# Kernel optimization log

Hardware: AMD Instinct MI355X
Metric: run time of the kernel (lower is better)

The kernel has to match this reference:

```python
import jax, jax.numpy as jnp
import numpy as np

DIM = 768
HEADS = 12
DH = DIM // HEADS  # 64


def setup_inputs() -> dict:
    key = jax.random.key(0)
    k1, k2, k3, k4, k5 = jax.random.split(key, 5)
    b, p = 16, 1024
    x = jax.random.normal(k1, (b, p, DIM), dtype=jnp.float32)
    # torch nn.Linear params: W [out, in], b [out]
    s_qkv = 1.0 / np.sqrt(DIM)
    Wqkv = jax.random.uniform(k2, (3 * DIM, DIM), jnp.float32, -s_qkv, s_qkv)
    bqkv = jax.random.uniform(k3, (3 * DIM,), jnp.float32, -s_qkv, s_qkv)
    Wo = jax.random.uniform(k4, (DIM, DIM), jnp.float32, -s_qkv, s_qkv)
    bo = jax.random.uniform(k5, (DIM,), jnp.float32, -s_qkv, s_qkv)
    return {"x": x, "Wqkv": Wqkv, "bqkv": bqkv, "Wo": Wo, "bo": bo}


def reference(x, Wqkv, bqkv, Wo, bo):
    b, p, _ = x.shape
    qkv = x @ Wqkv.T + bqkv                      # [b, p, 3*dim]
    q, k, v = jnp.split(qkv, 3, axis=-1)
    def to_heads(t):
        return t.reshape(b, p, HEADS, DH).transpose(0, 2, 1, 3)  # [b, h, p, d]
    q, k, v = to_heads(q), to_heads(k), to_heads(v)
    A = jnp.einsum('bhqd,bhkd->bhqk', q, k) / jnp.sqrt(jnp.float32(DH))
    # NOTE: softmax over the QUERY axis (dim=2), not the key axis
    P = jax.nn.softmax(A, axis=2)                # [b, h, q, k]
    MSA = jnp.einsum('bhqk,bhkd->bhqd', P, v)    # [b, h, p, d]
    MSA = MSA.transpose(0, 2, 1, 3).reshape(b, p, DIM)
    return MSA @ Wo.T + bo
```

## Files before the change

### kernel.cpp

```cpp
#include <hip/hip_runtime.h>
#include <hip/hip_bf16.h>
#include <math.h>

#define DIMC 768
#define HEADS 12
#define DHD 64
#define NB 16
#define NP 1024
#define NQKV (3*DIMC)

typedef __attribute__((ext_vector_type(8))) short bf16x8;
typedef __attribute__((ext_vector_type(4))) float f32x4;

__device__ __forceinline__ short f2bf(float f){
  unsigned u = __builtin_bit_cast(unsigned, f);
  u = (u + 0x7fffu + ((u >> 16) & 1u)) >> 16;
  return (short)u;
}
__device__ __forceinline__ float bf2f(short s){
  return __builtin_bit_cast(float, ((unsigned)(unsigned short)s) << 16);
}
__device__ __forceinline__ bf16x8 cvt8(float4 a, float4 b){
  bf16x8 v;
  v[0]=f2bf(a.x); v[1]=f2bf(a.y); v[2]=f2bf(a.z); v[3]=f2bf(a.w);
  v[4]=f2bf(b.x); v[5]=f2bf(b.y); v[6]=f2bf(b.z); v[7]=f2bf(b.w);
  return v;
}
__device__ __forceinline__ void glds16(const void* gsrc, void* ldst){
  __builtin_amdgcn_global_load_lds(
      (const __attribute__((address_space(1))) unsigned int*)gsrc,
      (__attribute__((address_space(3))) unsigned int*)ldst, 16, 0, 0);
}

__global__ __launch_bounds__(256) void cvt_bf16(const float* __restrict__ in, short* __restrict__ out, int n8)
{
  int i = blockIdx.x*256 + threadIdx.x;
  if (i < n8) {
    float4 f0 = ((const float4*)in)[i*2];
    float4 f1 = ((const float4*)in)[i*2+1];
    ((bf16x8*)out)[i] = cvt8(f0, f1);
  }
}

template<int BCVT, int OUTBF16>
__global__ __launch_bounds__(256) void gemm_bt(
    const short* __restrict__ A, const void* __restrict__ Bp,
    const float* __restrict__ bias, void* __restrict__ Cp,
    int N, int K)
{
  __shared__ __align__(16) short As[128*32];
  __shared__ __align__(16) short Bs[128*32];
  const int bn = blockIdx.x * 128, bm = blockIdx.y * 128;
  const int t = threadIdx.x;
  const int lane = t & 63, w = t >> 6;
  const int wr = w >> 1, wc = w & 1;
  const int lr = lane & 15, lg = lane >> 4;
  const int srow = lane >> 2;
  const int acol = (lane & 3) * 8;

  f32x4 acc[4][4] = {};

  for (int k0 = 0; k0 < K; k0 += 32) {
    glds16(A + (size_t)(bm + w*32 +  0 + srow)*K + k0 + acol, &As[(w*32 +  0)*32]);
    glds16(A + (size_t)(bm + w*32 + 16 + srow)*K + k0 + acol, &As[(w*32 + 16)*32]);
    if (BCVT) {
      const float* wp = (const float*)Bp + (size_t)(bn + (t>>1))*K + k0 + (t&1)*16;
      float4 f0 = ((const float4*)wp)[0];
      float4 f1 = ((const float4*)wp)[1];
      float4 f2 = ((const float4*)wp)[2];
      float4 f3 = ((const float4*)wp)[3];
      *(bf16x8*)&Bs[(t>>1)*32 + (t&1)*16]     = cvt8(f0, f1);
      *(bf16x8*)&Bs[(t>>1)*32 + (t&1)*16 + 8] = cvt8(f2, f3);
    } else {
      const short* bq = (const short*)Bp;
      glds16(bq + (size_t)(bn + w*32 +  0 + srow)*K + k0 + acol, &Bs[(w*32 +  0)*32]);
      glds16(bq + (size_t)(bn + w*32 + 16 + srow)*K + k0 + acol, &Bs[(w*32 + 16)*32]);
    }
    __syncthreads();
    bf16x8 a[4], b[4];
    #pragma unroll
    for (int i=0;i<4;i++) a[i] = *(const bf16x8*)&As[(wr*64 + i*16 + lr)*32 + lg*8];
    #pragma unroll
    for (int i=0;i<4;i++) b[i] = *(const bf16x8*)&Bs[(wc*64 + i*16 + lr)*32 + lg*8];
    #pragma unroll
    for (int mf=0;mf<4;mf++)
      #pragma unroll
      for (int nf=0;nf<4;nf++)
        acc[mf][nf] = __builtin_amdgcn_mfma_f32_16x16x32_bf16(a[mf], b[nf], acc[mf][nf], 0,0,0);
    __syncthreads();
  }
  #pragma unroll
  for (int nf=0;nf<4;nf++){
    const int n = bn + wc*64 + nf*16 + lr;
    const float bb = bias[n];
    #pragma unroll
    for (int mf=0;mf<4;mf++)
      #pragma unroll
      for (int i=0;i<4;i++){
        const int m = bm + wr*64 + mf*16 + lg*4 + i;
        const float v = acc[mf][nf][i] + bb;
        if (OUTBF16) ((short*)Cp)[(size_t)m*N + n] = f2bf(v);
        else         ((float*)Cp)[(size_t)m*N + n] = v;
      }
  }
}

__global__ __launch_bounds__(256) void vtrans(const short* __restrict__ qkv,
                                              const float* __restrict__ invs,
                                              short* __restrict__ vT)
{
  __shared__ __align__(16) short Ts[64][72];
  __shared__ float invl[64];
  const int pt = blockIdx.x, h = blockIdx.y, b = blockIdx.z;
  const int t = threadIdx.x;
  const size_t bh = (size_t)(b*HEADS + h);
  if (t < 64) invl[t] = invs[bh*NP + pt*64 + t];
  {
    const int r = t >> 2, q = t & 3;
    const short* src = qkv + (size_t)(b*NP + pt*64 + r)*NQKV + 2*DIMC + h*DHD + q*16;
    *(bf16x8*)&Ts[r][q*16]   = *(const bf16x8*)src;
    *(bf16x8*)&Ts[r][q*16+8] = *(const bf16x8*)(src+8);
  }
  __syncthreads();
  {
    const int d = t >> 2, q = t & 3;
    __align__(16) short tmp[16];
    #pragma unroll
    for (int j=0;j<16;j++) tmp[j] = f2bf(bf2f(Ts[q*16 + j][d]) * invl[q*16 + j]);
    short* dst = vT + (bh*DHD + d)*NP + pt*64 + q*16;
    *(bf16x8*)dst     = *(bf16x8*)&tmp[0];
    *(bf16x8*)(dst+8) = *(bf16x8*)&tmp[8];
  }
}

__global__ __launch_bounds__(256) void col_stats(const short* __restrict__ qkv, float* __restrict__ invs)
{
  __shared__ __align__(16) short Ks[128][72];
  __shared__ __align__(16) short Qs[64][72];
  __shared__ float red[4][128];
  const int kc = blockIdx.x, h = blockIdx.y, b = blockIdx.z;
  const int t = threadIdx.x;
  const int lane = t & 63, w = t >> 6;
  const int lr = lane & 15, lg = lane >> 4, lk = lg*8;
  const size_t rowbase = (size_t)(b*NP)*NQKV + h*DHD;
  {
    const int r = t >> 1, half = t & 1;
    const short* src = qkv + rowbase + (size_t)(kc*128 + r)*NQKV + DIMC + half*32;
    #pragma unroll
    for (int c=0;c<4;c++)
      *(bf16x8*)&Ks[r][half*32 + c*8] = *(const bf16x8*)(src + c*8);
  }
  float rsum[8] = {};
  for (int qt=0; qt<16; qt++){
    __syncthreads();
    {
      const int r = t >> 2, q = t & 3;
      const short* src = qkv + rowbase + (size_t)(qt*64 + r)*NQKV + q*16;
      *(bf16x8*)&Qs[r][q*16]   = *(const bf16x8*)src;
      *(bf16x8*)&Qs[r][q*16+8] = *(const bf16x8*)(src+8);
    }
    __syncthreads();
    bf16x8 qa0 = *(const bf16x8*)&Qs[w*16 + lr][lk];
    bf16x8 qa1 = *(const bf16x8*)&Qs[w*16 + lr][32 + lk];
    #pragma unroll
    for (int kf=0; kf<8; kf++){
      f32x4 acc = {};
      bf16x8 kb0 = *(const bf16x8*)&Ks[kf*16 + lr][lk];
      bf16x8 kb1 = *(const bf16x8*)&Ks[kf*16 + lr][32 + lk];
      acc = __builtin_amdgcn_mfma_f32_16x16x32_bf16(qa0, kb0, acc, 0,0,0);
      acc = __builtin_amdgcn_mfma_f32_16x16x32_bf16(qa1, kb1, acc, 0,0,0);
      #pragma unroll
      for (int i=0;i<4;i++) rsum[kf] += __expf(acc[i] * 0.125f);
    }
  }
  #pragma unroll
  for (int kf=0;kf<8;kf++){
    float v = rsum[kf];
    v += __shfl_xor(v, 16);
    v += __shfl_xor(v, 32);
    if (lane < 16) red[w][kf*16 + lr] = v;
  }
  __syncthreads();
  if (t < 128) {
    float s = red[0][t] + red[1][t] + red[2][t] + red[3][t];
    invs[(size_t)(b*HEADS + h)*NP + kc*128 + t] = 1.0f / s;
  }
}

__global__ __launch_bounds__(256) void attn_pv(const short* __restrict__ qkv, const short* __restrict__ vT,
                                               short* __restrict__ msa)
{
  __shared__ __align__(16) short Qs[64][72];
  __shared__ __align__(16) short Ks[64][72];
  __shared__ __align__(16) short Vs[64][72];
  __shared__ __align__(16) short Ps[4][16][72];
  const int qt = blockIdx.x, h = blockIdx.y, b = blockIdx.z;
  const int t = threadIdx.x;
  const int lane = t & 63, w = t >> 6;
  const int lr = lane & 15, lg = lane >> 4, lk = lg*8;
  const size_t qkvbase = (size_t)(b*NP)*NQKV + h*DHD;
  const size_t bh = (size_t)(b*HEADS + h);
  {
    const int r = t >> 2, q = t & 3;
    const short* src = qkv + qkvbase + (size_t)(qt*64 + r)*NQKV + q*16;
    *(bf16x8*)&Qs[r][q*16]   = *(const bf16x8*)src;
    *(bf16x8*)&Qs[r][q*16+8] = *(const bf16x8*)(src+8);
  }
  __syncthreads();
  bf16x8 qa0 = *(const bf16x8*)&Qs[w*16 + lr][lk];
  bf16x8 qa1 = *(const bf16x8*)&Qs[w*16 + lr][32 + lk];
  f32x4 o[4] = {};
  for (int kt=0; kt<16; kt++){
    __syncthreads();
    {
      const int r = t >> 2, q = t & 3;
      const short* ksrc = qkv + qkvbase + (size_t)(kt*64 + r)*NQKV + DIMC + q*16;
      *(bf16x8*)&Ks[r][q*16]   = *(const bf16x8*)ksrc;
      *(bf16x8*)&Ks[r][q*16+8] = *(const bf16x8*)(ksrc+8);
      const short* vsrc = vT + (bh*DHD + r)*NP + kt*64 + q*16;
      *(bf16x8*)&Vs[r][q*16]   = *(const bf16x8*)vsrc;
      *(bf16x8*)&Vs[r][q*16+8] = *(const bf16x8*)(vsrc+8);
    }
    __syncthreads();
    f32x4 s[4];
    #pragma unroll
    for (int kf=0;kf<4;kf++){
      f32x4 a = {};
      bf16x8 kb0 = *(const bf16x8*)&Ks[kf*16 + lr][lk];
      bf16x8 kb1 = *(const bf16x8*)&Ks[kf*16 + lr][32 + lk];
      a = __builtin_amdgcn_mfma_f32_16x16x32_bf16(qa0, kb0, a, 0,0,0);
      a = __builtin_amdgcn_mfma_f32_16x16x32_bf16(qa1, kb1, a, 0,0,0);
      s[kf] = a;
    }
    #pragma unroll
    for (int kf=0;kf<4;kf++){
      #pragma unroll
      for (int i=0;i<4;i++){
        const float p = __expf(s[kf][i]*0.125f);
        Ps[w][lg*4 + i][kf*16 + lr] = f2bf(p);
      }
    }
    __syncthreads();
    bf16x8 pa0 = *(const bf16x8*)&Ps[w][lr][lk];
    bf16x8 pa1 = *(const bf16x8*)&Ps[w][lr][32 + lk];
    #pragma unroll
    for (int df=0;df<4;df++){
      bf16x8 vb0 = *(const bf16x8*)&Vs[df*16 + lr][lk];
      bf16x8 vb1 = *(const bf16x8*)&Vs[df*16 + lr][32 + lk];
      o[df] = __builtin_amdgcn_mfma_f32_16x16x32_bf16(pa0, vb0, o[df], 0,0,0);
      o[df] = __builtin_amdgcn_mfma_f32_16x16x32_bf16(pa1, vb1, o[df], 0,0,0);
    }
  }
  #pragma unroll
  for (int df=0;df<4;df++){
    const int d = h*DHD + df*16 + lr;
    #pragma unroll
    for (int i=0;i<4;i++){
      const int p = qt*64 + w*16 + lg*4 + i;
      msa[((size_t)(b*NP) + p)*DIMC + d] = f2bf(o[df][i]);
    }
  }
}

extern "C" void kernel_launch(void* const* d_in, const int* in_sizes, int n_in,
                              void* d_out, int out_size, void* d_ws, size_t ws_size,
                              hipStream_t stream)
{
  const float* x    = (const float*)d_in[0];
  const float* Wqkv = (const float*)d_in[1];
  const float* bqkv = (const float*)d_in[2];
  const float* Wo   = (const float*)d_in[3];
  const float* bo   = (const float*)d_in[4];
  char* ws = (char*)d_ws;
  short* qkv   = (short*)ws;
  short* vT    = (short*)(ws + 75497472);
  short* Wqkvb = vT;
  short* msa   = (short*)(ws + 100663296);
  short* xb    = msa;
  float* invs  = (float*)(ws + 125829120);

  cvt_bf16<<<6144, 256, 0, stream>>>(x, xb, (16384*768)/8);
  cvt_bf16<<<864, 256, 0, stream>>>(Wqkv, Wqkvb, (2304*768)/8);
  gemm_bt<0,1><<<dim3(18, 128), 256, 0, stream>>>(xb, Wqkvb, bqkv, qkv, NQKV, DIMC);
  col_stats<<<dim3(8, HEADS, NB), 256, 0, stream>>>(qkv, invs);
  vtrans<<<dim3(16, HEADS, NB), 256, 0, stream>>>(qkv, invs, vT);
  attn_pv<<<dim3(16, HEADS, NB), 256, 0, stream>>>(qkv, vT, msa);
  gemm_bt<1,0><<<dim3(6, 128), 256, 0, stream>>>(msa, Wo, bo, d_out, DIMC, DIMC);
}
```

Measured before the change: 416.7 us.

## Fold softmax scale into Q, swizzle blocks across XCDs, double query tile in attn_pv

The QKV GEMM epilogue now multiplies Q by log2(e)/8, so the attention kernels use exp2f directly instead of a scaled __expf. All the main kernels use 1D grids with an XCD-aware swizzle so neighbouring tiles share L2. attn_pv now handles 128 queries per block, two 16-row groups per wave, which halves K/V tile loads per query. It also drops a __syncthreads between the P write and read, since each wave only touches its own Ps slice. Folding the scale into Q before bf16 rounding slightly changes numerics.

```diff
diff --git a/kernel.cpp b/kernel.cpp
--- a/kernel.cpp
+++ b/kernel.cpp
@@ -31,6 +31,9 @@
       (const __attribute__((address_space(1))) unsigned int*)gsrc,
       (__attribute__((address_space(3))) unsigned int*)ldst, 16, 0, 0);
 }
+__device__ __forceinline__ int xcd_swz(int p, int nwg){
+  return (p & 7) * (nwg >> 3) + (p >> 3);
+}
 
 __global__ __launch_bounds__(256) void cvt_bf16(const float* __restrict__ in, short* __restrict__ out, int n8)
 {
@@ -42,15 +45,16 @@
   }
 }
 
-template<int BCVT, int OUTBF16>
+template<int BCVT, int OUTBF16, int QSCALE>
 __global__ __launch_bounds__(256) void gemm_bt(
     const short* __restrict__ A, const void* __restrict__ Bp,
     const float* __restrict__ bias, void* __restrict__ Cp,
-    int N, int K)
+    int N, int K, int NX)
 {
   __shared__ __align__(16) short As[128*32];
   __shared__ __align__(16) short Bs[128*32];
-  const int bn = blockIdx.x * 128, bm = blockIdx.y * 128;
+  const int l = xcd_swz(blockIdx.x, gridDim.x);
+  const int bn = (l % NX) * 128, bm = (l / NX) * 128;
   const int t = threadIdx.x;
   const int lane = t & 63, w = t >> 6;
   const int wr = w >> 1, wc = w & 1;
@@ -93,12 +97,13 @@
   for (int nf=0;nf<4;nf++){
     const int n = bn + wc*64 + nf*16 + lr;
     const float bb = bias[n];
+    const float sc = (QSCALE && n < DIMC) ? 0.18033688011112042f : 1.0f;
     #pragma unroll
     for (int mf=0;mf<4;mf++)
       #pragma unroll
       for (int i=0;i<4;i++){
         const int m = bm + wr*64 + mf*16 + lg*4 + i;
-        const float v = acc[mf][nf][i] + bb;
+        const float v = (acc[mf][nf][i] + bb) * sc;
         if (OUTBF16) ((short*)Cp)[(size_t)m*N + n] = f2bf(v);
         else         ((float*)Cp)[(size_t)m*N + n] = v;
       }
@@ -138,7 +143,8 @@
   __shared__ __align__(16) short Ks[128][72];
   __shared__ __align__(16) short Qs[64][72];
   __shared__ float red[4][128];
-  const int kc = blockIdx.x, h = blockIdx.y, b = blockIdx.z;
+  const int l = xcd_swz(blockIdx.x, gridDim.x);
+  const int kc = l & 7, h = (l >> 3) % HEADS, b = l / (8*HEADS);
   const int t = threadIdx.x;
   const int lane = t & 63, w = t >> 6;
   const int lr = lane & 15, lg = lane >> 4, lk = lg*8;
@@ -170,7 +176,7 @@
       acc = __builtin_amdgcn_mfma_f32_16x16x32_bf16(qa0, kb0, acc, 0,0,0);
       acc = __builtin_amdgcn_mfma_f32_16x16x32_bf16(qa1, kb1, acc, 0,0,0);
       #pragma unroll
-      for (int i=0;i<4;i++) rsum[kf] += __expf(acc[i] * 0.125f);
+      for (int i=0;i<4;i++) rsum[kf] += exp2f(acc[i]);
     }
   }
   #pragma unroll
@@ -190,26 +196,33 @@
 __global__ __launch_bounds__(256) void attn_pv(const short* __restrict__ qkv, const short* __restrict__ vT,
                                                short* __restrict__ msa)
 {
-  __shared__ __align__(16) short Qs[64][72];
+  __shared__ __align__(16) short Qs[128][72];
   __shared__ __align__(16) short Ks[64][72];
   __shared__ __align__(16) short Vs[64][72];
   __shared__ __align__(16) short Ps[4][16][72];
-  const int qt = blockIdx.x, h = blockIdx.y, b = blockIdx.z;
+  const int l = xcd_swz(blockIdx.x, gridDim.x);
+  const int qt2 = l & 7, h = (l >> 3) % HEADS, b = l / (8*HEADS);
   const int t = threadIdx.x;
   const int lane = t & 63, w = t >> 6;
   const int lr = lane & 15, lg = lane >> 4, lk = lg*8;
   const size_t qkvbase = (size_t)(b*NP)*NQKV + h*DHD;
   const size_t bh = (size_t)(b*HEADS + h);
   {
-    const int r = t >> 2, q = t & 3;
-    const short* src = qkv + qkvbase + (size_t)(qt*64 + r)*NQKV + q*16;
-    *(bf16x8*)&Qs[r][q*16]   = *(const bf16x8*)src;
-    *(bf16x8*)&Qs[r][q*16+8] = *(const bf16x8*)(src+8);
+    const int r = t >> 1, half = t & 1;
+    const short* src = qkv + qkvbase + (size_t)(qt2*128 + r)*NQKV + half*32;
+    *(bf16x8*)&Qs[r][half*32]     = *(const bf16x8*)src;
+    *(bf16x8*)&Qs[r][half*32 + 8] = *(const bf16x8*)(src+8);
+    *(bf16x8*)&Qs[r][half*32 +16] = *(const bf16x8*)(src+16);
+    *(bf16x8*)&Qs[r][half*32 +24] = *(const bf16x8*)(src+24);
   }
   __syncthreads();
-  bf16x8 qa0 = *(const bf16x8*)&Qs[w*16 + lr][lk];
-  bf16x8 qa1 = *(const bf16x8*)&Qs[w*16 + lr][32 + lk];
-  f32x4 o[4] = {};
+  bf16x8 qa[2][2];
+  #pragma unroll
+  for (int g=0; g<2; g++){
+    qa[g][0] = *(const bf16x8*)&Qs[w*32 + g*16 + lr][lk];
+    qa[g][1] = *(const bf16x8*)&Qs[w*32 + g*16 + lr][32 + lk];
+  }
+  f32x4 o[2][4] = {};
   for (int kt=0; kt<16; kt++){
     __syncthreads();
     {
@@ -222,44 +235,45 @@
       *(bf16x8*)&Vs[r][q*16+8] = *(const bf16x8*)(vsrc+8);
     }
     __syncthreads();
-    f32x4 s[4];
-    #pragma unroll
-    for (int kf=0;kf<4;kf++){
-      f32x4 a = {};
-      bf16x8 kb0 = *(const bf16x8*)&Ks[kf*16 + lr][lk];
-      bf16x8 kb1 = *(const bf16x8*)&Ks[kf*16 + lr][32 + lk];
-      a = __builtin_amdgcn_mfma_f32_16x16x32_bf16(qa0, kb0, a, 0,0,0);
-      a = __builtin_amdgcn_mfma_f32_16x16x32_bf16(qa1, kb1, a, 0,0,0);
-      s[kf] = a;
-    }
-    #pragma unroll
-    for (int kf=0;kf<4;kf++){
+    #pragma unroll
+    for (int g=0; g<2; g++){
+      f32x4 s[4];
+      #pragma unroll
+      for (int kf=0;kf<4;kf++){
+        f32x4 a = {};
+        bf16x8 kb0 = *(const bf16x8*)&Ks[kf*16 + lr][lk];
+        bf16x8 kb1 = *(const bf16x8*)&Ks[kf*16 + lr][32 + lk];
+        a = __builtin_amdgcn_mfma_f32_16x16x32_bf16(qa[g][0], kb0, a, 0,0,0);
+        a = __builtin_amdgcn_mfma_f32_16x16x32_bf16(qa[g][1], kb1, a, 0,0,0);
+        s[kf] = a;
+      }
+      #pragma unroll
+      for (int kf=0;kf<4;kf++)
+        #pragma unroll
+        for (int i=0;i<4;i++)
+          Ps[w][lg*4 + i][kf*16 + lr] = f2bf(exp2f(s[kf][i]));
+      bf16x8 pa0 = *(const bf16x8*)&Ps[w][lr][lk];
+      bf16x8 pa1 = *(const bf16x8*)&Ps[w][lr][32 + lk];
+      #pragma unroll
+      for (int df=0;df<4;df++){
+        bf16x8 vb0 = *(const bf16x8*)&Vs[df*16 + lr][lk];
+        bf16x8 vb1 = *(const bf16x8*)&Vs[df*16 + lr][32 + lk];
+        o[g][df] = __builtin_amdgcn_mfma_f32_16x16x32_bf16(pa0, vb0, o[g][df], 0,0,0);
+        o[g][df] = __builtin_amdgcn_mfma_f32_16x16x32_bf16(pa1, vb1, o[g][df], 0,0,0);
+      }
+    }
+  }
+  #pragma unroll
+  for (int g=0; g<2; g++)
+    #pragma unroll
+    for (int df=0;df<4;df++){
+      const int d = h*DHD + df*16 + lr;
       #pragma unroll
       for (int i=0;i<4;i++){
-        const float p = __expf(s[kf][i]*0.125f);
-        Ps[w][lg*4 + i][kf*16 + lr] = f2bf(p);
+        const int p = qt2*128 + w*32 + g*16 + lg*4 + i;
+        msa[((size_t)(b*NP) + p)*DIMC + d] = f2bf(o[g][df][i]);
       }
     }
-    __syncthreads();
-    bf16x8 pa0 = *(const bf16x8*)&Ps[w][lr][lk];
-    bf16x8 pa1 = *(const bf16x8*)&Ps[w][lr][32 + lk];
-    #pragma unroll
-    for (int df=0;df<4;df++){
-      bf16x8 vb0 = *(const bf16x8*)&Vs[df*16 + lr][lk];
-      bf16x8 vb1 = *(const bf16x8*)&Vs[df*16 + lr][32 + lk];
-      o[df] = __builtin_amdgcn_mfma_f32_16x16x32_bf16(pa0, vb0, o[df], 0,0,0);
-      o[df] = __builtin_amdgcn_mfma_f32_16x16x32_bf16(pa1, vb1, o[df], 0,0,0);
-    }
-  }
-  #pragma unroll
-  for (int df=0;df<4;df++){
-    const int d = h*DHD + df*16 + lr;
-    #pragma unroll
-    for (int i=0;i<4;i++){
-      const int p = qt*64 + w*16 + lg*4 + i;
-      msa[((size_t)(b*NP) + p)*DIMC + d] = f2bf(o[df][i]);
-    }
-  }
 }
 
 extern "C" void kernel_launch(void* const* d_in, const int* in_sizes, int n_in,
@@ -281,9 +295,9 @@
 
   cvt_bf16<<<6144, 256, 0, stream>>>(x, xb, (16384*768)/8);
   cvt_bf16<<<864, 256, 0, stream>>>(Wqkv, Wqkvb, (2304*768)/8);
-  gemm_bt<0,1><<<dim3(18, 128), 256, 0, stream>>>(xb, Wqkvb, bqkv, qkv, NQKV, DIMC);
-  col_stats<<<dim3(8, HEADS, NB), 256, 0, stream>>>(qkv, invs);
+  gemm_bt<0,1,1><<<2304, 256, 0, stream>>>(xb, Wqkvb, bqkv, qkv, NQKV, DIMC, 18);
+  col_stats<<<1536, 256, 0, stream>>>(qkv, invs);
   vtrans<<<dim3(16, HEADS, NB), 256, 0, stream>>>(qkv, invs, vT);
-  attn_pv<<<dim3(16, HEADS, NB), 256, 0, stream>>>(qkv, vT, msa);
-  gemm_bt<1,0><<<dim3(6, 128), 256, 0, stream>>>(msa, Wo, bo, d_out, DIMC, DIMC);
-}
+  attn_pv<<<1536, 256, 0, stream>>>(qkv, vT, msa);
+  gemm_bt<1,0,0><<<768, 256, 0, stream>>>(msa, Wo, bo, d_out, DIMC, DIMC, 6);
+}
```

Result: faster. 408.2 us (-2.0%).
